# Performance work log

Hardware: AMD Instinct MI355X
Metric: run time of the kernel (lower is better)

Reference implementation:

```python
import jax, jax.numpy as jnp
import numpy as np

# db2 decomposition low-pass filter (pywt dec_lo)
DEC_LO = np.array([-0.12940952255092145, 0.22414386804185735,
                    0.8365163037378079, 0.48296291314469025], dtype=np.float32)
FILT_LEN = 4


def _dwt_lo_last_axis(x):
    """Single-level db2 low-pass + downsample along the last axis of NCHW x,
    matching pywt.dwt (mode='symmetric'): symmetric-pad by L-1, full-like
    convolution, keep odd output positions -> length floor((n+L-1)/2)."""
    L = FILT_LEN
    C = x.shape[1]
    # np.convolve flips the filter; lax.conv does correlation, so pre-flip.
    k = jnp.asarray(DEC_LO[::-1].copy(), dtype=x.dtype)
    ker = jnp.tile(k.reshape(1, 1, 1, L), (C, 1, 1, 1))  # depthwise OIHW
    xp = jnp.pad(x, ((0, 0), (0, 0), (0, 0), (L - 1, L - 1)), mode='symmetric')
    xp = xp[..., 1:]  # offset so stride-2 valid conv picks positions 1,3,5,...
    return jax.lax.conv_general_dilated(
        xp, ker, window_strides=(1, 2), padding='VALID',
        feature_group_count=C,
        dimension_numbers=('NCHW', 'OIHW', 'NCHW'))


def dwt_ll(x):
    """LL band of pywt.dwt2(x, 'db2') over the last two axes (separable)."""
    y = _dwt_lo_last_axis(x)                               # filter W axis
    y = _dwt_lo_last_axis(y.transpose(0, 1, 3, 2))         # filter H axis
    return y.transpose(0, 1, 3, 2)


def setup_inputs() -> dict:
    key = jax.random.key(0)
    x = jax.random.normal(key, (4, 64, 512, 512), dtype=jnp.float32)
    return {"x": x}


def reference(x):
    return dwt_ll(x)
```

## Files before the change

### kernel.cpp

```cpp
#include <hip/hip_runtime.h>


#define IN_H 512
#define IN_W 512
#define OUT_H 257
#define OUT_W 257

#define TW 64
#define TH 16
#define IW_T (2 * TW + 2)
#define IH_T (2 * TH + 2)
#define LDS_STRIDE (IW_T + 2)

__global__ __launch_bounds__(256, 2)
void dwt_ll_kernel(const float* __restrict__ x, float* __restrict__ out) {
    __shared__ float tile[IH_T][LDS_STRIDE];

    const int tid = threadIdx.x;
    const int jw0 = blockIdx.x * TW;
    const int jh0 = blockIdx.y * TH;
    const int plane = blockIdx.z;

    const float* __restrict__ xp = x + (size_t)plane * (IN_H * IN_W);
    float* __restrict__ op = out + (size_t)plane * (OUT_H * OUT_W);

    const int rbase = 2 * jh0 - 2;
    const int cbase = 2 * jw0 - 2;

    for (int idx = tid; idx < IH_T * IW_T; idx += 256) {
        int r = idx / IW_T;
        int c = idx - r * IW_T;
        int gr = rbase + r;
        int gc = cbase + c;
        gr = (gr < 0) ? (-gr - 1) : gr;
        gr = (gr >= IN_H) ? (2 * IN_H - 1 - gr) : gr;
        gc = (gc < 0) ? (-gc - 1) : gc;
        gc = (gc >= IN_W) ? (2 * IN_W - 1 - gc) : gc;
        tile[r][c] = xp[gr * IN_W + gc];
    }
    __syncthreads();

    const float g0 = 0.48296291314469025f;
    const float g1 = 0.8365163037378079f;
    const float g2 = 0.22414386804185735f;
    const float g3 = -0.12940952255092145f;

    const int tx = tid & 63;
    const int ty = tid >> 6;
    const int ow = jw0 + tx;
    if (ow >= OUT_W) return;

    const int cc = 2 * tx;
    const int r0 = 8 * ty;

    float h[10];
#pragma unroll
    for (int r = 0; r < 10; ++r) {
        const float2 a = *(const float2*)&tile[r0 + r][cc];
        const float2 b = *(const float2*)&tile[r0 + r][cc + 2];
        h[r] = g0 * a.x + g1 * a.y + g2 * b.x + g3 * b.y;
    }

#pragma unroll
    for (int k = 0; k < 4; ++k) {
        const int oh = jh0 + ty * 4 + k;
        if (oh < OUT_H) {
            const float v = g0 * h[2 * k] + g1 * h[2 * k + 1]
                          + g2 * h[2 * k + 2] + g3 * h[2 * k + 3];
            op[oh * OUT_W + ow] = v;
        }
    }
}

extern "C" void kernel_launch(void* const* d_in, const int* in_sizes, int n_in,
                              void* d_out, int out_size, void* d_ws, size_t ws_size,
                              hipStream_t stream) {
    const float* x = (const float*)d_in[0];
    float* out = (float*)d_out;

    dim3 grid((OUT_W + TW - 1) / TW, (OUT_H + TH - 1) / TH, 4 * 64);
    dim3 block(256);
    dwt_ll_kernel<<<grid, block, 0, stream>>>(x, out);
}
```

Baseline: 382.9 us.

## Use full-width row strips with float4 loads and separate column-halo fill

Each block now covers full-width strips of 8 output rows (18 input rows by 512 columns) instead of 64x16 tiles. Interior loads become aligned float4 reads with no per-element column mirroring, and a small set of threads fills the symmetric left and right halo columns separately. This cuts the halo overfetch between horizontal neighbours and the per-element index arithmetic, and occupancy hints rise to 4 blocks per CU. In exchange there is more vertical halo overhead (18 rows loaded per 8 output rows), and the 256 threads cover 257 output columns, so one thread runs a second iteration.

```diff
diff --git a/kernel.cpp b/kernel.cpp
--- a/kernel.cpp
+++ b/kernel.cpp
@@ -5,38 +5,48 @@
 #define IN_W 512
 #define OUT_H 257
 #define OUT_W 257
+#define TH 8
+#define NROWS (2 * TH + 2)
+#define TSTRIDE 520
 
-#define TW 64
-#define TH 16
-#define IW_T (2 * TW + 2)
-#define IH_T (2 * TH + 2)
-#define LDS_STRIDE (IW_T + 2)
-
-__global__ __launch_bounds__(256, 2)
+__global__ __launch_bounds__(256, 4)
 void dwt_ll_kernel(const float* __restrict__ x, float* __restrict__ out) {
-    __shared__ float tile[IH_T][LDS_STRIDE];
+    __shared__ __align__(16) float tile[NROWS][TSTRIDE];
 
     const int tid = threadIdx.x;
-    const int jw0 = blockIdx.x * TW;
-    const int jh0 = blockIdx.y * TH;
-    const int plane = blockIdx.z;
+    const int by = blockIdx.x;
+    const int plane = blockIdx.y;
 
     const float* __restrict__ xp = x + (size_t)plane * (IN_H * IN_W);
     float* __restrict__ op = out + (size_t)plane * (OUT_H * OUT_W);
 
-    const int rbase = 2 * jh0 - 2;
-    const int cbase = 2 * jw0 - 2;
+    const int rbase = 2 * (TH * by) - 2;
 
-    for (int idx = tid; idx < IH_T * IW_T; idx += 256) {
-        int r = idx / IW_T;
-        int c = idx - r * IW_T;
+#pragma unroll
+    for (int i = 0; i < 9; ++i) {
+        const int idx = tid + i * 256;
+        const int r = idx >> 7;
+        const int c4 = (idx & 127) << 2;
         int gr = rbase + r;
-        int gc = cbase + c;
         gr = (gr < 0) ? (-gr - 1) : gr;
         gr = (gr >= IN_H) ? (2 * IN_H - 1 - gr) : gr;
-        gc = (gc < 0) ? (-gc - 1) : gc;
-        gc = (gc >= IN_W) ? (2 * IN_W - 1 - gc) : gc;
-        tile[r][c] = xp[gr * IN_W + gc];
+        const float4 v = *(const float4*)&xp[gr * IN_W + c4];
+        *(float4*)&tile[r][4 + c4] = v;
+    }
+
+    if (tid < 8 * NROWS) {
+        const int r = tid >> 3;
+        const int e = tid & 7;
+        const int tcol = (e < 4) ? e : (512 + e);
+        float v = 0.0f;
+        if (e >= 2) {
+            const int scol = (e < 4) ? (3 - e) : (515 - e);
+            int gr = rbase + r;
+            gr = (gr < 0) ? (-gr - 1) : gr;
+            gr = (gr >= IN_H) ? (2 * IN_H - 1 - gr) : gr;
+            v = xp[gr * IN_W + scol];
+        }
+        tile[r][tcol] = v;
     }
     __syncthreads();
 
@@ -45,29 +55,22 @@
     const float g2 = 0.22414386804185735f;
     const float g3 = -0.12940952255092145f;
 
-    const int tx = tid & 63;
-    const int ty = tid >> 6;
-    const int ow = jw0 + tx;
-    if (ow >= OUT_W) return;
-
-    const int cc = 2 * tx;
-    const int r0 = 8 * ty;
-
-    float h[10];
+    for (int ow = tid; ow < OUT_W; ow += 256) {
+        const int cc = 2 * ow + 2;
+        float h[NROWS];
 #pragma unroll
-    for (int r = 0; r < 10; ++r) {
-        const float2 a = *(const float2*)&tile[r0 + r][cc];
-        const float2 b = *(const float2*)&tile[r0 + r][cc + 2];
-        h[r] = g0 * a.x + g1 * a.y + g2 * b.x + g3 * b.y;
-    }
-
+        for (int r = 0; r < NROWS; ++r) {
+            const float2 a = *(const float2*)&tile[r][cc];
+            const float2 b = *(const float2*)&tile[r][cc + 2];
+            h[r] = g0 * a.x + g1 * a.y + g2 * b.x + g3 * b.y;
+        }
 #pragma unroll
-    for (int k = 0; k < 4; ++k) {
-        const int oh = jh0 + ty * 4 + k;
-        if (oh < OUT_H) {
-            const float v = g0 * h[2 * k] + g1 * h[2 * k + 1]
-                          + g2 * h[2 * k + 2] + g3 * h[2 * k + 3];
-            op[oh * OUT_W + ow] = v;
+        for (int k = 0; k < TH; ++k) {
+            const int oh = TH * by + k;
+            if (oh < OUT_H) {
+                op[oh * OUT_W + ow] = g0 * h[2 * k] + g1 * h[2 * k + 1]
+                                    + g2 * h[2 * k + 2] + g3 * h[2 * k + 3];
+            }
         }
     }
 }
@@ -78,7 +81,7 @@
     const float* x = (const float*)d_in[0];
     float* out = (float*)d_out;
 
-    dim3 grid((OUT_W + TW - 1) / TW, (OUT_H + TH - 1) / TH, 4 * 64);
+    dim3 grid((OUT_H + TH - 1) / TH, 4 * 64);
     dim3 block(256);
     dwt_ll_kernel<<<grid, block, 0, stream>>>(x, out);
 }
```

New measurement: 370.8 us. 1.03x faster.
